# Kernel optimization log

Hardware: AMD Instinct MI355X
Metric: run time of the kernel (lower is better)

The kernel has to match this reference:

```python
import jax, jax.numpy as jnp
import numpy as np

ENCODER_DIM, DECODER_DIM, ATTENTION_DIM = 2048, 512, 512
B, L = 128, 196


def setup_inputs() -> dict:
    key = jax.random.key(0)
    ks = jax.random.split(key, 8)
    s_u = 1.0 / np.sqrt(ENCODER_DIM)
    s_w = 1.0 / np.sqrt(DECODER_DIM)
    s_a = 1.0 / np.sqrt(ATTENTION_DIM)
    return {
        "features": jax.random.normal(ks[0], (B, L, ENCODER_DIM), jnp.float32),
        "hidden_state": jax.random.normal(ks[1], (B, DECODER_DIM), jnp.float32),
        "U_w": jax.random.uniform(ks[2], (ENCODER_DIM, ATTENTION_DIM), jnp.float32, -s_u, s_u),
        "U_b": jax.random.uniform(ks[3], (ATTENTION_DIM,), jnp.float32, -s_u, s_u),
        "W_w": jax.random.uniform(ks[4], (DECODER_DIM, ATTENTION_DIM), jnp.float32, -s_w, s_w),
        "W_b": jax.random.uniform(ks[5], (ATTENTION_DIM,), jnp.float32, -s_w, s_w),
        "A_w": jax.random.uniform(ks[6], (ATTENTION_DIM,), jnp.float32, -s_a, s_a),
        "A_b": jax.random.uniform(ks[7], (1,), jnp.float32, -s_a, s_a),
    }


def reference(features, hidden_state, U_w, U_b, W_w, W_b, A_w, A_b):
    # u_hs: [B, L, A], w_ah: [B, A]
    u_hs = jnp.einsum('ble,ea->bla', features, U_w) + U_b
    w_ah = hidden_state @ W_w + W_b
    combined = jnp.tanh(u_hs + w_ah[:, None, :])          # [B, L, A]
    scores = jnp.einsum('bla,a->bl', combined, A_w) + A_b[0]  # [B, L]
    alpha = jax.nn.softmax(scores, axis=1)                 # [B, L]
    context = jnp.einsum('bl,ble->be', alpha, features)    # [B, E]
    return alpha, context
```

## Files before the change

kernel.cpp:

```cpp
#include <hip/hip_runtime.h>
#include <hip/hip_bf16.h>

#define ENC 2048
#define ADIM 512
#define DEC 512
#define NBATCH 128
#define NL 196
#define MTOT (NBATCH * NL)

typedef __attribute__((ext_vector_type(8))) short short8;
typedef __attribute__((ext_vector_type(4))) float f32x4;

__device__ __forceinline__ unsigned short f2bf(float f) {
    __hip_bfloat16 h = __float2bfloat16(f);
    union { __hip_bfloat16 h; unsigned short u; } cv; cv.h = h; return cv.u;
}
__device__ __forceinline__ unsigned int f2bf2(float lo, float hi) {
    __hip_bfloat162 h = __float22bfloat162_rn(float2{lo, hi});
    union { __hip_bfloat162 h; unsigned int u; } cv; cv.h = h; return cv.u;
}

__device__ __forceinline__ void load_lds16(const void* g, void* l) {
    __builtin_amdgcn_global_load_lds(
        (const __attribute__((address_space(1))) unsigned int*)g,
        (__attribute__((address_space(3))) unsigned int*)l, 16, 0, 0);
}

__global__ void wah_kernel(const float* __restrict__ hidden, const float* __restrict__ Ww,
                           const float* __restrict__ Wb, float* __restrict__ wah) {
    __shared__ __align__(16) float hs[DEC];
    const int b = blockIdx.x, a = threadIdx.x;
    hs[a] = hidden[b * DEC + a];
    __syncthreads();
    float acc = Wb[a];
    #pragma unroll 4
    for (int d = 0; d < DEC; d += 4) {
        f32x4 h = *(const f32x4*)&hs[d];
        acc += h.x * Ww[(d    ) * ADIM + a];
        acc += h.y * Ww[(d + 1) * ADIM + a];
        acc += h.z * Ww[(d + 2) * ADIM + a];
        acc += h.w * Ww[(d + 3) * ADIM + a];
    }
    wah[b * ADIM + a] = acc;
}

__global__ void transpose_uw(const float* __restrict__ Uw, unsigned short* __restrict__ uwT) {
    __shared__ float t[32][33];
    const int k0 = blockIdx.x * 32, n0 = blockIdx.y * 32;
    const int tx = threadIdx.x, ty = threadIdx.y;
    #pragma unroll
    for (int i = 0; i < 4; ++i)
        t[ty + 8 * i][tx] = Uw[(size_t)(k0 + ty + 8 * i) * ADIM + n0 + tx];
    __syncthreads();
    #pragma unroll
    for (int i = 0; i < 4; ++i)
        uwT[(size_t)(n0 + ty + 8 * i) * ENC + k0 + tx] = f2bf(t[tx][ty + 8 * i]);
}

__global__ __launch_bounds__(256, 3) void gemm_score_kernel(
    const float* __restrict__ feat, const unsigned short* __restrict__ uwT,
    const float* __restrict__ Ub, const float* __restrict__ wahb,
    const float* __restrict__ Aw, float* __restrict__ part)
{
    __shared__ __align__(16) unsigned char As[32768];
    __shared__ __align__(16) unsigned char Bs[16384];

    const int tid  = threadIdx.x;
    const int lane = tid & 63;
    const int w    = tid >> 6;
    const int wr   = w >> 1, wc = w & 1;
    const int l15  = lane & 15, ldr = lane >> 4;

    const int bid  = blockIdx.x;
    const int work = (bid & 7) * 98 + (bid >> 3);
    const int mb   = work >> 2;
    const int nbk  = work & 3;

    const char* featb = (const char*)feat;
    const char* uwTb  = (const char*)uwT;
    const char* aSrc[8];
    #pragma unroll
    for (int c = 0; c < 8; ++c) {
        const int row   = w * 32 + c * 4 + ldr;
        const int inner = (l15 * 16) ^ (ldr << 5) ^ ((c & 1) << 4);
        aSrc[c] = featb + (size_t)(mb * 128 + row) * (ENC * 4) + inner;
    }
    const char* bSrc[4];
    #pragma unroll
    for (int c = 0; c < 4; ++c) {
        const int n     = w * 32 + c * 8 + (lane >> 3);
        const int inner = ((lane & 7) * 16) ^ (((lane >> 3) & 7) << 4);
        bSrc[c] = uwTb + (size_t)(nbk * 128 + n) * (ENC * 2) + inner;
    }
    unsigned char* aDst = As + w * 8192;
    unsigned char* bDst = Bs + w * 4096;

    const int sA = ((l15 & 3) << 5) | ((l15 & 4) << 2);
    int abyte[4][2][2], bbyte[4][2];
    #pragma unroll
    for (int f = 0; f < 4; ++f) {
        const int r = wr * 64 + f * 16 + l15;
        const int n = wc * 64 + f * 16 + l15;
        #pragma unroll
        for (int ks = 0; ks < 2; ++ks) {
            const int k4 = ks * 128 + ldr * 32;
            abyte[f][ks][0] = r * 256 + ((k4     ) ^ sA);
            abyte[f][ks][1] = r * 256 + ((k4 + 16) ^ sA);
            bbyte[f][ks]    = n * 128 + ((ks * 64 + ldr * 16) ^ ((n & 7) << 4));
        }
    }

    f32x4 acc[4][4];
    #pragma unroll
    for (int i = 0; i < 4; ++i)
        #pragma unroll
        for (int j = 0; j < 4; ++j)
            acc[i][j] = (f32x4){0.f, 0.f, 0.f, 0.f};

    #pragma unroll 1
    for (int kt = 0; kt < 32; ++kt) {
        __syncthreads();
        #pragma unroll
        for (int c = 0; c < 8; ++c)
            load_lds16(aSrc[c] + (size_t)kt * 256, aDst + c * 1024);
        #pragma unroll
        for (int c = 0; c < 4; ++c)
            load_lds16(bSrc[c] + (size_t)kt * 128, bDst + c * 1024);
        __syncthreads();

        #pragma unroll
        for (int ks = 0; ks < 2; ++ks) {
            short8 af[4], bf[4];
            #pragma unroll
            for (int f = 0; f < 4; ++f) {
                f32x4 lo = *(const f32x4*)(As + abyte[f][ks][0]);
                f32x4 hi = *(const f32x4*)(As + abyte[f][ks][1]);
                union { unsigned int u[4]; short8 s; } cv;
                cv.u[0] = f2bf2(lo.x, lo.y);
                cv.u[1] = f2bf2(lo.z, lo.w);
                cv.u[2] = f2bf2(hi.x, hi.y);
                cv.u[3] = f2bf2(hi.z, hi.w);
                af[f] = cv.s;
                bf[f] = *(const short8*)(Bs + bbyte[f][ks]);
            }
            #pragma unroll
            for (int fm = 0; fm < 4; ++fm)
                #pragma unroll
                for (int fn = 0; fn < 4; ++fn)
                    acc[fm][fn] = __builtin_amdgcn_mfma_f32_16x16x32_bf16(
                        af[fm], bf[fn], acc[fm][fn], 0, 0, 0);
        }
    }

    float ub4[4], aw4[4]; int cidx[4];
    #pragma unroll
    for (int f = 0; f < 4; ++f) {
        const int c = nbk * 128 + wc * 64 + f * 16 + l15;
        cidx[f] = c; ub4[f] = Ub[c]; aw4[f] = Aw[c];
    }
    #pragma unroll
    for (int fm = 0; fm < 4; ++fm) {
        #pragma unroll
        for (int r = 0; r < 4; ++r) {
            const int m = mb * 128 + wr * 64 + fm * 16 + ldr * 4 + r;
            const int b = m / NL;
            const float* wrow = wahb + b * ADIM;
            float s = 0.f;
            #pragma unroll
            for (int f = 0; f < 4; ++f)
                s += aw4[f] * tanhf(acc[fm][f][r] + ub4[f] + wrow[cidx[f]]);
            s += __shfl_xor(s, 1);
            s += __shfl_xor(s, 2);
            s += __shfl_xor(s, 4);
            s += __shfl_xor(s, 8);
            if (l15 == 0) part[(nbk * 2 + wc) * MTOT + m] = s;
        }
    }
}

__global__ void softmax_kernel(const float* __restrict__ part, const float* __restrict__ Ab,
                               float* __restrict__ alpha) {
    const int b = blockIdx.x, t = threadIdx.x;
    float sv = 0.f;
    if (t < NL) {
        sv = Ab[0];
        #pragma unroll
        for (int p = 0; p < 8; ++p) sv += part[p * MTOT + b * NL + t];
    }
    float v = (t < NL) ? sv : -3.4e38f;
    #pragma unroll
    for (int o = 32; o >= 1; o >>= 1) v = fmaxf(v, __shfl_xor(v, o));
    __shared__ float rm[4], rs[4];
    if ((t & 63) == 0) rm[t >> 6] = v;
    __syncthreads();
    const float bm = fmaxf(fmaxf(rm[0], rm[1]), fmaxf(rm[2], rm[3]));
    const float e = (t < NL) ? expf(sv - bm) : 0.f;
    float s = e;
    #pragma unroll
    for (int o = 32; o >= 1; o >>= 1) s += __shfl_xor(s, o);
    if ((t & 63) == 0) rs[t >> 6] = s;
    __syncthreads();
    const float bs = rs[0] + rs[1] + rs[2] + rs[3];
    if (t < NL) alpha[b * NL + t] = e / bs;
}

__global__ void context_kernel(const float* __restrict__ feat, const float* __restrict__ alpha,
                               float* __restrict__ ctx) {
    __shared__ float al[NL];
    const int b = blockIdx.x, chunk = blockIdx.y, t = threadIdx.x;
    for (int i = t; i < NL; i += 128) al[i] = alpha[b * NL + i];
    __syncthreads();
    const int e0 = chunk * 512 + t * 4;
    const float* fp = feat + (size_t)b * NL * ENC + e0;
    f32x4 acc0 = (f32x4){0.f, 0.f, 0.f, 0.f};
    f32x4 acc1 = (f32x4){0.f, 0.f, 0.f, 0.f};
    #pragma unroll 2
    for (int l = 0; l < NL; l += 2) {
        f32x4 f0 = *(const f32x4*)(fp + (size_t)l * ENC);
        f32x4 f1 = *(const f32x4*)(fp + (size_t)(l + 1) * ENC);
        acc0 += al[l] * f0;
        acc1 += al[l + 1] * f1;
    }
    f32x4 rsum = acc0 + acc1;
    *(f32x4*)(ctx + (size_t)b * ENC + e0) = rsum;
}

extern "C" void kernel_launch(void* const* d_in, const int* in_sizes, int n_in,
                              void* d_out, int out_size, void* d_ws, size_t ws_size,
                              hipStream_t stream) {
    const float* feat   = (const float*)d_in[0];
    const float* hidden = (const float*)d_in[1];
    const float* Uw     = (const float*)d_in[2];
    const float* Ub     = (const float*)d_in[3];
    const float* Ww     = (const float*)d_in[4];
    const float* Wb     = (const float*)d_in[5];
    const float* Aw     = (const float*)d_in[6];
    const float* Ab     = (const float*)d_in[7];

    float* out   = (float*)d_out;
    float* alpha = out;
    float* ctx   = out + MTOT;

    char* ws = (char*)d_ws;
    float*          wahb = (float*)ws;
    unsigned short* uwT  = (unsigned short*)(ws + 262144);
    float*          partb= (float*)(ws + 262144 + 2097152);

    wah_kernel<<<dim3(128), dim3(512), 0, stream>>>(hidden, Ww, Wb, wahb);
    transpose_uw<<<dim3(64, 16), dim3(32, 8), 0, stream>>>(Uw, uwT);
    gemm_score_kernel<<<dim3(784), dim3(256), 0, stream>>>(feat, uwT, Ub, wahb, Aw, partb);
    softmax_kernel<<<dim3(128), dim3(256), 0, stream>>>(partb, Ab, alpha);
    context_kernel<<<dim3(128, 4), dim3(128), 0, stream>>>(feat, alpha, ctx);
}
```

Baseline: 186.0 us.

## Double-buffer LDS tiles with halved K-step to overlap loads and MFMA

Switches the GEMM main loop from a single LDS buffer with K-tile 64 to two ping-pong buffers with K-tile 32, so the global-to-LDS loads for the next tile are issued before computing the current one. Swizzle patterns and address precomputation are redone for the narrower tiles. Total LDS per block stays the same, but there are twice as many barrier pairs per K and less work per stage. The intent is to hide global load latency behind MFMA work.

```diff
diff --git a/kernel.cpp b/kernel.cpp
--- a/kernel.cpp
+++ b/kernel.cpp
@@ -7,6 +7,7 @@
 #define NBATCH 128
 #define NL 196
 #define MTOT (NBATCH * NL)
+#define KT 64
 
 typedef __attribute__((ext_vector_type(8))) short short8;
 typedef __attribute__((ext_vector_type(4))) float f32x4;
@@ -62,8 +63,8 @@
     const float* __restrict__ Ub, const float* __restrict__ wahb,
     const float* __restrict__ Aw, float* __restrict__ part)
 {
-    __shared__ __align__(16) unsigned char As[32768];
-    __shared__ __align__(16) unsigned char Bs[16384];
+    __shared__ __align__(16) unsigned char As[2][16384];
+    __shared__ __align__(16) unsigned char Bs[2][8192];
 
     const int tid  = threadIdx.x;
     const int lane = tid & 63;
@@ -78,36 +79,35 @@
 
     const char* featb = (const char*)feat;
     const char* uwTb  = (const char*)uwT;
-    const char* aSrc[8];
-    #pragma unroll
-    for (int c = 0; c < 8; ++c) {
-        const int row   = w * 32 + c * 4 + ldr;
-        const int inner = (l15 * 16) ^ (ldr << 5) ^ ((c & 1) << 4);
-        aSrc[c] = featb + (size_t)(mb * 128 + row) * (ENC * 4) + inner;
-    }
-    const char* bSrc[4];
-    #pragma unroll
-    for (int c = 0; c < 4; ++c) {
-        const int n     = w * 32 + c * 8 + (lane >> 3);
-        const int inner = ((lane & 7) * 16) ^ (((lane >> 3) & 7) << 4);
-        bSrc[c] = uwTb + (size_t)(nbk * 128 + n) * (ENC * 2) + inner;
-    }
-    unsigned char* aDst = As + w * 8192;
-    unsigned char* bDst = Bs + w * 4096;
-
-    const int sA = ((l15 & 3) << 5) | ((l15 & 4) << 2);
-    int abyte[4][2][2], bbyte[4][2];
+    const char* aSrc[4];
+    {
+        const int innerA = ((lane & 7) * 16) ^ ((lane >> 3) << 4);
+        #pragma unroll
+        for (int c = 0; c < 4; ++c) {
+            const int row = w * 32 + c * 8 + (lane >> 3);
+            aSrc[c] = featb + (size_t)(mb * 128 + row) * (ENC * 4) + innerA;
+        }
+    }
+    const char* bSrc[2];
+    {
+        const int nn = (lane >> 2) & 7;
+        const int innerB = ((lane & 3) * 16) ^ ((nn & 3) << 4) ^ ((nn & 4) << 2);
+        #pragma unroll
+        for (int c = 0; c < 2; ++c) {
+            const int n = w * 32 + c * 16 + (lane >> 2);
+            bSrc[c] = uwTb + (size_t)(nbk * 128 + n) * (ENC * 2) + innerB;
+        }
+    }
+
+    int abyte[4][2], bbyte[4];
     #pragma unroll
     for (int f = 0; f < 4; ++f) {
-        const int r = wr * 64 + f * 16 + l15;
-        const int n = wc * 64 + f * 16 + l15;
-        #pragma unroll
-        for (int ks = 0; ks < 2; ++ks) {
-            const int k4 = ks * 128 + ldr * 32;
-            abyte[f][ks][0] = r * 256 + ((k4     ) ^ sA);
-            abyte[f][ks][1] = r * 256 + ((k4 + 16) ^ sA);
-            bbyte[f][ks]    = n * 128 + ((ks * 64 + ldr * 16) ^ ((n & 7) << 4));
-        }
+        const int r  = wr * 64 + f * 16 + l15;
+        const int n  = wc * 64 + f * 16 + l15;
+        const int rs = (l15 & 7) << 4;
+        abyte[f][0] = r * 128 + ((ldr * 32)      ^ rs);
+        abyte[f][1] = r * 128 + ((ldr * 32 + 16) ^ rs);
+        bbyte[f]    = n * 64  + ((ldr * 16) ^ ((l15 & 3) << 4) ^ ((l15 & 4) << 2));
     }
 
     f32x4 acc[4][4];
@@ -117,40 +117,49 @@
         for (int j = 0; j < 4; ++j)
             acc[i][j] = (f32x4){0.f, 0.f, 0.f, 0.f};
 
+#define STAGE(KTI, BB) {                                                         \
+    _Pragma("unroll")                                                            \
+    for (int c = 0; c < 4; ++c)                                                  \
+        load_lds16(aSrc[c] + (size_t)(KTI) * 128, &As[BB][w * 4096 + c * 1024]); \
+    _Pragma("unroll")                                                            \
+    for (int c = 0; c < 2; ++c)                                                  \
+        load_lds16(bSrc[c] + (size_t)(KTI) * 64,  &Bs[BB][w * 2048 + c * 1024]); \
+}
+#define COMPUTE(BB) {                                                            \
+    short8 af[4], bf[4];                                                         \
+    _Pragma("unroll")                                                            \
+    for (int f = 0; f < 4; ++f) {                                                \
+        f32x4 lo = *(const f32x4*)(As[BB] + abyte[f][0]);                        \
+        f32x4 hi = *(const f32x4*)(As[BB] + abyte[f][1]);                        \
+        union { unsigned int u[4]; short8 s; } cv;                               \
+        cv.u[0] = f2bf2(lo.x, lo.y);                                             \
+        cv.u[1] = f2bf2(lo.z, lo.w);                                             \
+        cv.u[2] = f2bf2(hi.x, hi.y);                                             \
+        cv.u[3] = f2bf2(hi.z, hi.w);                                             \
+        af[f] = cv.s;                                                            \
+        bf[f] = *(const short8*)(Bs[BB] + bbyte[f]);                             \
+    }                                                                            \
+    _Pragma("unroll")                                                            \
+    for (int fm = 0; fm < 4; ++fm)                                               \
+        _Pragma("unroll")                                                        \
+        for (int fn = 0; fn < 4; ++fn)                                           \
+            acc[fm][fn] = __builtin_amdgcn_mfma_f32_16x16x32_bf16(               \
+                af[fm], bf[fn], acc[fm][fn], 0, 0, 0);                           \
+}
+
+    STAGE(0, 0);
+    __syncthreads();
     #pragma unroll 1
-    for (int kt = 0; kt < 32; ++kt) {
+    for (int kt = 0; kt < KT; kt += 2) {
+        if (kt + 1 < KT) STAGE(kt + 1, 1);
+        COMPUTE(0);
         __syncthreads();
-        #pragma unroll
-        for (int c = 0; c < 8; ++c)
-            load_lds16(aSrc[c] + (size_t)kt * 256, aDst + c * 1024);
-        #pragma unroll
-        for (int c = 0; c < 4; ++c)
-            load_lds16(bSrc[c] + (size_t)kt * 128, bDst + c * 1024);
+        if (kt + 2 < KT) STAGE(kt + 2, 0);
+        COMPUTE(1);
         __syncthreads();
-
-        #pragma unroll
-        for (int ks = 0; ks < 2; ++ks) {
-            short8 af[4], bf[4];
-            #pragma unroll
-            for (int f = 0; f < 4; ++f) {
-                f32x4 lo = *(const f32x4*)(As + abyte[f][ks][0]);
-                f32x4 hi = *(const f32x4*)(As + abyte[f][ks][1]);
-                union { unsigned int u[4]; short8 s; } cv;
-                cv.u[0] = f2bf2(lo.x, lo.y);
-                cv.u[1] = f2bf2(lo.z, lo.w);
-                cv.u[2] = f2bf2(hi.x, hi.y);
-                cv.u[3] = f2bf2(hi.z, hi.w);
-                af[f] = cv.s;
-                bf[f] = *(const short8*)(Bs + bbyte[f][ks]);
-            }
-            #pragma unroll
-            for (int fm = 0; fm < 4; ++fm)
-                #pragma unroll
-                for (int fn = 0; fn < 4; ++fn)
-                    acc[fm][fn] = __builtin_amdgcn_mfma_f32_16x16x32_bf16(
-                        af[fm], bf[fn], acc[fm][fn], 0, 0, 0);
-        }
-    }
+    }
+#undef STAGE
+#undef COMPUTE
 
     float ub4[4], aw4[4]; int cidx[4];
     #pragma unroll
```

Result: slower. 202.4 us (+8.8%).

## Double-buffer GEMM mainloop with register-staged A conversion and prefetch

Applied to the files above, without the earlier changes.

Restructures the score GEMM mainloop from a single-buffer BK=64 loop into a two-stage, double-buffered pipeline with BK=32. Features are now loaded into registers, converted to bf16 once, and written to LDS as bf16, so A occupies half the shared memory and is not reconverted by each wave. U_w tiles still arrive through direct global-to-LDS loads, and both operands are prefetched two steps ahead using manual waitcnt and barriers. The intent is to hide global load latency behind MFMA work and cut LDS traffic and repeated conversion. In exchange it adds more barriers per K step, depends on hand-tuned vmcnt counts, and raises register pressure from the staged A data.

```diff
diff --git a/kernel.cpp b/kernel.cpp
--- a/kernel.cpp
+++ b/kernel.cpp
@@ -7,9 +7,11 @@
 #define NBATCH 128
 #define NL 196
 #define MTOT (NBATCH * NL)
+#define NKT 64
 
 typedef __attribute__((ext_vector_type(8))) short short8;
 typedef __attribute__((ext_vector_type(4))) float f32x4;
+typedef __attribute__((ext_vector_type(4))) unsigned int u32x4;
 
 __device__ __forceinline__ unsigned short f2bf(float f) {
     __hip_bfloat16 h = __float2bfloat16(f);
@@ -62,8 +64,10 @@
     const float* __restrict__ Ub, const float* __restrict__ wahb,
     const float* __restrict__ Aw, float* __restrict__ part)
 {
-    __shared__ __align__(16) unsigned char As[32768];
-    __shared__ __align__(16) unsigned char Bs[16384];
+    __shared__ __align__(16) unsigned char Ab0[8192];
+    __shared__ __align__(16) unsigned char Ab1[8192];
+    __shared__ __align__(16) unsigned char Bb0[8192];
+    __shared__ __align__(16) unsigned char Bb1[8192];
 
     const int tid  = threadIdx.x;
     const int lane = tid & 63;
@@ -76,38 +80,24 @@
     const int mb   = work >> 2;
     const int nbk  = work & 3;
 
-    const char* featb = (const char*)feat;
-    const char* uwTb  = (const char*)uwT;
-    const char* aSrc[8];
-    #pragma unroll
-    for (int c = 0; c < 8; ++c) {
-        const int row   = w * 32 + c * 4 + ldr;
-        const int inner = (l15 * 16) ^ (ldr << 5) ^ ((c & 1) << 4);
-        aSrc[c] = featb + (size_t)(mb * 128 + row) * (ENC * 4) + inner;
-    }
-    const char* bSrc[4];
-    #pragma unroll
-    for (int c = 0; c < 4; ++c) {
-        const int n     = w * 32 + c * 8 + (lane >> 3);
-        const int inner = ((lane & 7) * 16) ^ (((lane >> 3) & 7) << 4);
-        bSrc[c] = uwTb + (size_t)(nbk * 128 + n) * (ENC * 2) + inner;
-    }
-    unsigned char* aDst = As + w * 8192;
-    unsigned char* bDst = Bs + w * 4096;
-
-    const int sA = ((l15 & 3) << 5) | ((l15 & 4) << 2);
-    int abyte[4][2][2], bbyte[4][2];
+    const int r_ = tid >> 1, h_ = tid & 1;
+    const float* aSrc = feat + (size_t)(mb * 128 + r_) * ENC + h_ * 16;
+    const int xw = (r_ >> 1) & 3;
+    const int wA0 = r_ * 64 + (((h_ * 2 + 0) ^ xw) << 4);
+    const int wA1 = r_ * 64 + (((h_ * 2 + 1) ^ xw) << 4);
+
+    const unsigned short* bSrc = uwT
+        + (size_t)(nbk * 128 + w * 32 + (lane >> 2)) * ENC
+        + ((lane & 3) ^ ((lane >> 3) & 3)) * 8;
+
+    const int xr = (l15 >> 1) & 3;
+    int abyte[4], bbyte[4];
     #pragma unroll
     for (int f = 0; f < 4; ++f) {
         const int r = wr * 64 + f * 16 + l15;
         const int n = wc * 64 + f * 16 + l15;
-        #pragma unroll
-        for (int ks = 0; ks < 2; ++ks) {
-            const int k4 = ks * 128 + ldr * 32;
-            abyte[f][ks][0] = r * 256 + ((k4     ) ^ sA);
-            abyte[f][ks][1] = r * 256 + ((k4 + 16) ^ sA);
-            bbyte[f][ks]    = n * 128 + ((ks * 64 + ldr * 16) ^ ((n & 7) << 4));
-        }
+        abyte[f] = r * 64 + ((ldr ^ xr) << 4);
+        bbyte[f] = n * 64 + ((ldr ^ xr) << 4);
     }
 
     f32x4 acc[4][4];
@@ -117,40 +107,72 @@
         for (int j = 0; j < 4; ++j)
             acc[i][j] = (f32x4){0.f, 0.f, 0.f, 0.f};
 
+    f32x4 a00, a01, a02, a03;
+    f32x4 a10, a11, a12, a13;
+
+#define ISSUE_A(KTI, R0, R1, R2, R3) {                                  \
+    const f32x4* p = (const f32x4*)(aSrc + (size_t)(KTI) * 32);         \
+    R0 = p[0]; R1 = p[1]; R2 = p[2]; R3 = p[3];                         \
+    __builtin_amdgcn_sched_barrier(0);                                  \
+}
+#define ISSUE_B(KTI, BB) {                                              \
+    load_lds16(bSrc + (size_t)(KTI) * 32,            (BB) + w * 2048);  \
+    load_lds16(bSrc + 16 * ENC + (size_t)(KTI) * 32, (BB) + w * 2048 + 1024); \
+    __builtin_amdgcn_sched_barrier(0);                                  \
+}
+#define CVT_WRITE(R0, R1, R2, R3, AB) {                                 \
+    u32x4 w0, w1;                                                       \
+    w0.x = f2bf2(R0.x, R0.y); w0.y = f2bf2(R0.z, R0.w);                 \
+    w0.z = f2bf2(R1.x, R1.y); w0.w = f2bf2(R1.z, R1.w);                 \
+    w1.x = f2bf2(R2.x, R2.y); w1.y = f2bf2(R2.z, R2.w);                 \
+    w1.z = f2bf2(R3.x, R3.y); w1.w = f2bf2(R3.z, R3.w);                 \
+    *(u32x4*)((AB) + wA0) = w0;                                         \
+    *(u32x4*)((AB) + wA1) = w1;                                         \
+}
+#define COMPUTE(AB, BB) {                                               \
+    short8 af[4], bf[4];                                                \
+    _Pragma("unroll")                                                   \
+    for (int f = 0; f < 4; ++f) {                                       \
+        af[f] = *(const short8*)((AB) + abyte[f]);                      \
+        bf[f] = *(const short8*)((BB) + bbyte[f]);                      \
+    }                                                                   \
+    _Pragma("unroll")                                                   \
+    for (int fm = 0; fm < 4; ++fm)                                      \
+        _Pragma("unroll")                                               \
+        for (int fn = 0; fn < 4; ++fn)                                  \
+            acc[fm][fn] = __builtin_amdgcn_mfma_f32_16x16x32_bf16(      \
+                af[fm], bf[fn], acc[fm][fn], 0, 0, 0);                  \
+}
+#define PHASE(T2, RA0, RA1, RA2, RA3, AB, BB) {                         \
+    CVT_WRITE(RA0, RA1, RA2, RA3, AB);                                  \
+    ISSUE_A(T2, RA0, RA1, RA2, RA3);                                    \
+    asm volatile("s_waitcnt vmcnt(10)");                                \
+    __builtin_amdgcn_sched_barrier(0);                                  \
+    asm volatile("s_waitcnt lgkmcnt(0)");                               \
+    __builtin_amdgcn_sched_barrier(0);                                  \
+    __builtin_amdgcn_s_barrier();                                       \
+    COMPUTE(AB, BB);                                                    \
+    __builtin_amdgcn_s_barrier();                                       \
+    ISSUE_B(T2, BB);                                                    \
+}
+
+    ISSUE_A(0, a00, a01, a02, a03);
+    ISSUE_B(0, Bb0);
+    ISSUE_A(1, a10, a11, a12, a13);
+    ISSUE_B(1, Bb1);
+
     #pragma unroll 1
-    for (int kt = 0; kt < 32; ++kt) {
-        __syncthreads();
-        #pragma unroll
-        for (int c = 0; c < 8; ++c)
-            load_lds16(aSrc[c] + (size_t)kt * 256, aDst + c * 1024);
-        #pragma unroll
-        for (int c = 0; c < 4; ++c)
-            load_lds16(bSrc[c] + (size_t)kt * 128, bDst + c * 1024);
-        __syncthreads();
-
-        #pragma unroll
-        for (int ks = 0; ks < 2; ++ks) {
-            short8 af[4], bf[4];
-            #pragma unroll
-            for (int f = 0; f < 4; ++f) {
-                f32x4 lo = *(const f32x4*)(As + abyte[f][ks][0]);
-                f32x4 hi = *(const f32x4*)(As + abyte[f][ks][1]);
-                union { unsigned int u[4]; short8 s; } cv;
-                cv.u[0] = f2bf2(lo.x, lo.y);
-                cv.u[1] = f2bf2(lo.z, lo.w);
-                cv.u[2] = f2bf2(hi.x, hi.y);
-                cv.u[3] = f2bf2(hi.z, hi.w);
-                af[f] = cv.s;
-                bf[f] = *(const short8*)(Bs + bbyte[f][ks]);
-            }
-            #pragma unroll
-            for (int fm = 0; fm < 4; ++fm)
-                #pragma unroll
-                for (int fn = 0; fn < 4; ++fn)
-                    acc[fm][fn] = __builtin_amdgcn_mfma_f32_16x16x32_bf16(
-                        af[fm], bf[fn], acc[fm][fn], 0, 0, 0);
-        }
-    }
+    for (int kt = 0; kt < NKT; kt += 2) {
+        const int k2 = (kt + 2 < NKT) ? kt + 2 : NKT - 1;
+        const int k3 = (kt + 3 < NKT) ? kt + 3 : NKT - 1;
+        PHASE(k2, a00, a01, a02, a03, Ab0, Bb0);
+        PHASE(k3, a10, a11, a12, a13, Ab1, Bb1);
+    }
+#undef ISSUE_A
+#undef ISSUE_B
+#undef CVT_WRITE
+#undef COMPUTE
+#undef PHASE
 
     float ub4[4], aw4[4]; int cidx[4];
     #pragma unroll
```

Result: faster. 176.8 us (-5.0%).

## Convert A tile to bf16 once in registers and halve GEMM M-tile

Applied to the files above, without the earlier changes.

The score GEMM now loads fp32 feature rows through registers, converts them to bf16 once, and stores bf16 tiles into a swizzled LDS buffer. Before, each wave converted fp32 operands on every LDS fragment read. The M-tile drops from 128 to 64 rows with each wave owning 32 columns, which doubles the grid, shrinks LDS use, and raises the occupancy target to 4 blocks. The partial-score buffer grows from 8 to 32 slices and softmax sums more partials. Each block now reuses the feature tile across fewer columns, and the A loads are synchronous register loads rather than direct-to-LDS loads.

```diff
diff --git a/kernel.cpp b/kernel.cpp
--- a/kernel.cpp
+++ b/kernel.cpp
@@ -7,9 +7,12 @@
 #define NBATCH 128
 #define NL 196
 #define MTOT (NBATCH * NL)
+#define NKT 32
+#define NPART 32
 
 typedef __attribute__((ext_vector_type(8))) short short8;
 typedef __attribute__((ext_vector_type(4))) float f32x4;
+typedef __attribute__((ext_vector_type(4))) unsigned int u32x4;
 
 __device__ __forceinline__ unsigned short f2bf(float f) {
     __hip_bfloat16 h = __float2bfloat16(f);
@@ -57,123 +60,107 @@
         uwT[(size_t)(n0 + ty + 8 * i) * ENC + k0 + tx] = f2bf(t[tx][ty + 8 * i]);
 }
 
-__global__ __launch_bounds__(256, 3) void gemm_score_kernel(
+__global__ __launch_bounds__(256, 4) void gemm_score_kernel(
     const float* __restrict__ feat, const unsigned short* __restrict__ uwT,
     const float* __restrict__ Ub, const float* __restrict__ wahb,
     const float* __restrict__ Aw, float* __restrict__ part)
 {
-    __shared__ __align__(16) unsigned char As[32768];
+    __shared__ __align__(16) unsigned char As[8192];
     __shared__ __align__(16) unsigned char Bs[16384];
 
     const int tid  = threadIdx.x;
     const int lane = tid & 63;
     const int w    = tid >> 6;
-    const int wr   = w >> 1, wc = w & 1;
     const int l15  = lane & 15, ldr = lane >> 4;
 
     const int bid  = blockIdx.x;
-    const int work = (bid & 7) * 98 + (bid >> 3);
+    const int work = (bid & 7) * 196 + (bid >> 3);
     const int mb   = work >> 2;
     const int nbk  = work & 3;
 
-    const char* featb = (const char*)feat;
-    const char* uwTb  = (const char*)uwT;
-    const char* aSrc[8];
-    #pragma unroll
-    for (int c = 0; c < 8; ++c) {
-        const int row   = w * 32 + c * 4 + ldr;
-        const int inner = (l15 * 16) ^ (ldr << 5) ^ ((c & 1) << 4);
-        aSrc[c] = featb + (size_t)(mb * 128 + row) * (ENC * 4) + inner;
-    }
-    const char* bSrc[4];
-    #pragma unroll
-    for (int c = 0; c < 4; ++c) {
-        const int n     = w * 32 + c * 8 + (lane >> 3);
-        const int inner = ((lane & 7) * 16) ^ (((lane >> 3) & 7) << 4);
-        bSrc[c] = uwTb + (size_t)(nbk * 128 + n) * (ENC * 2) + inner;
-    }
-    unsigned char* aDst = As + w * 8192;
-    unsigned char* bDst = Bs + w * 4096;
-
-    const int sA = ((l15 & 3) << 5) | ((l15 & 4) << 2);
-    int abyte[4][2][2], bbyte[4][2];
-    #pragma unroll
-    for (int f = 0; f < 4; ++f) {
-        const int r = wr * 64 + f * 16 + l15;
-        const int n = wc * 64 + f * 16 + l15;
+    const int r_ = tid >> 2, kq = tid & 3;
+    const float* aSrc = feat + (size_t)(mb * 64 + r_) * ENC + kq * 16;
+    const int wA0 = r_ * 128 + (((kq * 2    ) ^ (r_ & 7)) << 4);
+    const int wA1 = r_ * 128 + (((kq * 2 + 1) ^ (r_ & 7)) << 4);
+
+    const unsigned short* bSrc = uwT
+        + (size_t)(nbk * 128 + w * 32 + (lane >> 3)) * ENC
+        + (((lane & 7) ^ ((lane >> 3) & 7)) << 3);
+
+    int abyte[4][2], bbyte[2][2];
+    #pragma unroll
+    for (int ks = 0; ks < 2; ++ks) {
+        const int sl = ((ks * 4 + ldr) ^ (l15 & 7)) << 4;
+        #pragma unroll
+        for (int f = 0; f < 4; ++f)
+            abyte[f][ks] = (f * 16 + l15) * 128 + sl;
+        #pragma unroll
+        for (int g = 0; g < 2; ++g)
+            bbyte[g][ks] = (w * 32 + g * 16 + l15) * 128 + sl;
+    }
+
+    f32x4 acc[4][2];
+    #pragma unroll
+    for (int i = 0; i < 4; ++i)
+        #pragma unroll
+        for (int j = 0; j < 2; ++j)
+            acc[i][j] = (f32x4){0.f, 0.f, 0.f, 0.f};
+
+    #pragma unroll 1
+    for (int kt = 0; kt < NKT; ++kt) {
+        const f32x4* p = (const f32x4*)(aSrc + (size_t)kt * 64);
+        f32x4 a0 = p[0], a1 = p[1], a2 = p[2], a3 = p[3];
+        #pragma unroll
+        for (int c = 0; c < 4; ++c)
+            load_lds16(bSrc + (size_t)kt * 64 + c * 8 * ENC, Bs + w * 4096 + c * 1024);
+        u32x4 w0, w1;
+        w0.x = f2bf2(a0.x, a0.y); w0.y = f2bf2(a0.z, a0.w);
+        w0.z = f2bf2(a1.x, a1.y); w0.w = f2bf2(a1.z, a1.w);
+        w1.x = f2bf2(a2.x, a2.y); w1.y = f2bf2(a2.z, a2.w);
+        w1.z = f2bf2(a3.x, a3.y); w1.w = f2bf2(a3.z, a3.w);
+        *(u32x4*)(As + wA0) = w0;
+        *(u32x4*)(As + wA1) = w1;
+        __syncthreads();
+
         #pragma unroll
         for (int ks = 0; ks < 2; ++ks) {
-            const int k4 = ks * 128 + ldr * 32;
-            abyte[f][ks][0] = r * 256 + ((k4     ) ^ sA);
-            abyte[f][ks][1] = r * 256 + ((k4 + 16) ^ sA);
-            bbyte[f][ks]    = n * 128 + ((ks * 64 + ldr * 16) ^ ((n & 7) << 4));
-        }
-    }
-
-    f32x4 acc[4][4];
-    #pragma unroll
-    for (int i = 0; i < 4; ++i)
-        #pragma unroll
-        for (int j = 0; j < 4; ++j)
-            acc[i][j] = (f32x4){0.f, 0.f, 0.f, 0.f};
-
-    #pragma unroll 1
-    for (int kt = 0; kt < 32; ++kt) {
-        __syncthreads();
-        #pragma unroll
-        for (int c = 0; c < 8; ++c)
-            load_lds16(aSrc[c] + (size_t)kt * 256, aDst + c * 1024);
-        #pragma unroll
-        for (int c = 0; c < 4; ++c)
-            load_lds16(bSrc[c] + (size_t)kt * 128, bDst + c * 1024);
-        __syncthreads();
-
-        #pragma unroll
-        for (int ks = 0; ks < 2; ++ks) {
-            short8 af[4], bf[4];
-            #pragma unroll
-            for (int f = 0; f < 4; ++f) {
-                f32x4 lo = *(const f32x4*)(As + abyte[f][ks][0]);
-                f32x4 hi = *(const f32x4*)(As + abyte[f][ks][1]);
-                union { unsigned int u[4]; short8 s; } cv;
-                cv.u[0] = f2bf2(lo.x, lo.y);
-                cv.u[1] = f2bf2(lo.z, lo.w);
-                cv.u[2] = f2bf2(hi.x, hi.y);
-                cv.u[3] = f2bf2(hi.z, hi.w);
-                af[f] = cv.s;
-                bf[f] = *(const short8*)(Bs + bbyte[f][ks]);
-            }
+            short8 af[4], bf[2];
+            #pragma unroll
+            for (int f = 0; f < 4; ++f) af[f] = *(const short8*)(As + abyte[f][ks]);
+            #pragma unroll
+            for (int g = 0; g < 2; ++g) bf[g] = *(const short8*)(Bs + bbyte[g][ks]);
             #pragma unroll
             for (int fm = 0; fm < 4; ++fm)
                 #pragma unroll
-                for (int fn = 0; fn < 4; ++fn)
-                    acc[fm][fn] = __builtin_amdgcn_mfma_f32_16x16x32_bf16(
-                        af[fm], bf[fn], acc[fm][fn], 0, 0, 0);
+                for (int g = 0; g < 2; ++g)
+                    acc[fm][g] = __builtin_amdgcn_mfma_f32_16x16x32_bf16(
+                        af[fm], bf[g], acc[fm][g], 0, 0, 0);
         }
-    }
-
-    float ub4[4], aw4[4]; int cidx[4];
-    #pragma unroll
-    for (int f = 0; f < 4; ++f) {
-        const int c = nbk * 128 + wc * 64 + f * 16 + l15;
-        cidx[f] = c; ub4[f] = Ub[c]; aw4[f] = Aw[c];
+        __syncthreads();
+    }
+
+    float ub2[2], aw2[2]; int cidx[2];
+    #pragma unroll
+    for (int g = 0; g < 2; ++g) {
+        const int c = nbk * 128 + w * 32 + g * 16 + l15;
+        cidx[g] = c; ub2[g] = Ub[c]; aw2[g] = Aw[c];
     }
     #pragma unroll
     for (int fm = 0; fm < 4; ++fm) {
         #pragma unroll
         for (int r = 0; r < 4; ++r) {
-            const int m = mb * 128 + wr * 64 + fm * 16 + ldr * 4 + r;
+            const int m = mb * 64 + fm * 16 + ldr * 4 + r;
             const int b = m / NL;
             const float* wrow = wahb + b * ADIM;
-            float s = 0.f;
-            #pragma unroll
-            for (int f = 0; f < 4; ++f)
-                s += aw4[f] * tanhf(acc[fm][f][r] + ub4[f] + wrow[cidx[f]]);
-            s += __shfl_xor(s, 1);
-            s += __shfl_xor(s, 2);
-            s += __shfl_xor(s, 4);
-            s += __shfl_xor(s, 8);
-            if (l15 == 0) part[(nbk * 2 + wc) * MTOT + m] = s;
+            #pragma unroll
+            for (int g = 0; g < 2; ++g) {
+                float s = aw2[g] * tanhf(acc[fm][g][r] + ub2[g] + wrow[cidx[g]]);
+                s += __shfl_xor(s, 1);
+                s += __shfl_xor(s, 2);
+                s += __shfl_xor(s, 4);
+                s += __shfl_xor(s, 8);
+                if (l15 == 0) part[(nbk * 8 + w * 2 + g) * MTOT + m] = s;
+            }
         }
     }
 }
@@ -184,8 +171,8 @@
     float sv = 0.f;
     if (t < NL) {
         sv = Ab[0];
-        #pragma unroll
-        for (int p = 0; p < 8; ++p) sv += part[p * MTOT + b * NL + t];
+        #pragma unroll 8
+        for (int p = 0; p < NPART; ++p) sv += part[p * MTOT + b * NL + t];
     }
     float v = (t < NL) ? sv : -3.4e38f;
     #pragma unroll
@@ -248,7 +235,7 @@
 
     wah_kernel<<<dim3(128), dim3(512), 0, stream>>>(hidden, Ww, Wb, wahb);
     transpose_uw<<<dim3(64, 16), dim3(32, 8), 0, stream>>>(Uw, uwT);
-    gemm_score_kernel<<<dim3(784), dim3(256), 0, stream>>>(feat, uwT, Ub, wahb, Aw, partb);
+    gemm_score_kernel<<<dim3(1568), dim3(256), 0, stream>>>(feat, uwT, Ub, wahb, Aw, partb);
     softmax_kernel<<<dim3(128), dim3(256), 0, stream>>>(partb, Ab, alpha);
     context_kernel<<<dim3(128, 4), dim3(128), 0, stream>>>(feat, alpha, ctx);
 }
```

Measured after the change: 169.8 us. 1.1x faster.
